# Kernel optimization log

Hardware: AMD Instinct MI355X
Metric: run time of the kernel (lower is better)

The kernel has to match this reference:

```python
import jax, jax.numpy as jnp
import numpy as np

N_NODES = 50000
N_GRAPHS = 128
IN_DIM = 512
HID = 512
N_LAYERS = 3


def setup_inputs() -> dict:
    key = jax.random.key(0)
    ks = jax.random.split(key, 12)
    inp = {
        "x": jax.random.normal(ks[0], (N_NODES, IN_DIM), dtype=jnp.float32),
        "walk2": jax.random.randint(ks[1], (3, N_NODES), 0, N_NODES, dtype=jnp.int32),
        "walk3": jax.random.randint(ks[2], (4, N_NODES), 0, N_NODES, dtype=jnp.int32),
        "walk4": jax.random.randint(ks[3], (5, N_NODES), 0, N_NODES, dtype=jnp.int32),
        "batch": jnp.sort(jax.random.randint(ks[4], (N_NODES,), 0, N_GRAPHS, dtype=jnp.int32)),
    }
    dims = [IN_DIM, HID, HID]
    for i in range(N_LAYERS):
        scale = 1.0 / np.sqrt(dims[i])
        inp[f"W{i}"] = jax.random.normal(ks[5 + i], (dims[i], HID), dtype=jnp.float32) * scale
        inp[f"b{i}"] = jnp.zeros((HID,), dtype=jnp.float32)
    return inp


def _gather_sum(z, walk):
    # walk: [L, N] node indices -> sum of gathered embeddings, [N, H]
    L, N = walk.shape
    return jnp.take(z, walk.reshape(-1), axis=0).reshape(L, N, z.shape[1]).sum(0)


def reference(x, walk2, walk3, walk4, batch, W0, b0, W1, b1, W2, b2):
    layers = [(W0, b0), (W1, b1), (W2, b2)]
    path_batch = jnp.take(batch, walk2[0])  # [N]
    counts = jax.ops.segment_sum(jnp.ones((path_batch.shape[0],), jnp.float32),
                                 path_batch, num_segments=N_GRAPHS)
    denom = jnp.maximum(counts, 1.0)[:, None]  # avoid div-by-zero for empty graphs
    z = x
    g = []
    for W, b in layers:
        z = z @ W + b  # [N, H]
        path_emb = _gather_sum(z, walk2) + _gather_sum(z, walk3) + _gather_sum(z, walk4)
        pooled = jax.ops.segment_sum(path_emb, path_batch, num_segments=N_GRAPHS) / denom
        g.append(pooled)
    return jnp.concatenate(g, axis=1)  # [N_GRAPHS, 3*H]
```

## Files before the change

kernel.cpp:

```cpp
#include <hip/hip_runtime.h>

#define N_NODES 50000
#define N_GRAPHS 128
#define HID 512

#define KSPAN   272
#define NSTEP   17
#define KS2     48
#define KSPLIT  (KS2 * 4)
#define KPAD    (KSPAN * KSPLIT)
#define NPANEL  (KPAD / 16)

#define C8_OFF     0
#define C8_BYTES   ((size_t)N_GRAPHS * KPAD)
#define PSUM_OFF   (C8_OFF + C8_BYTES)
#define PSUM_BYTES ((size_t)N_GRAPHS * HID * 4)
#define COUNTS_OFF (PSUM_OFF + PSUM_BYTES)
#define ZERO_BYTES (COUNTS_OFF + 512)
#define APACK_OFF  ZERO_BYTES
#define APACK_BYTES ((size_t)NPANEL * 4 * 64 * 16)
#define PART_OFF   (APACK_OFF + APACK_BYTES)
#define PART_BYTES ((size_t)KS2 * N_GRAPHS * HID * 4)

typedef __attribute__((ext_vector_type(8))) short bf16x8;
typedef __attribute__((ext_vector_type(16))) float f32x16;

__global__ __launch_bounds__(256)
void build_c_kernel(const int* __restrict__ w2, const int* __restrict__ w3,
                    const int* __restrict__ w4, const int* __restrict__ batch,
                    unsigned int* __restrict__ C32, int* __restrict__ counts) {
    __shared__ int hist[N_GRAPHS];
    const int t = threadIdx.x;
    if (t < N_GRAPHS) hist[t] = 0;
    __syncthreads();
    const int i = blockIdx.x * 256 + t;
    if (i < N_NODES) {
        const int a = w2[i];
        const int g = batch[a];
        atomicAdd(&hist[g], 1);
        unsigned int* row = C32 + (size_t)g * (KPAD / 4);
        int nn[12];
        nn[0]  = a;
        nn[1]  = w2[N_NODES + i];
        nn[2]  = w2[2 * N_NODES + i];
        nn[3]  = w3[i];
        nn[4]  = w3[N_NODES + i];
        nn[5]  = w3[2 * N_NODES + i];
        nn[6]  = w3[3 * N_NODES + i];
        nn[7]  = w4[i];
        nn[8]  = w4[N_NODES + i];
        nn[9]  = w4[2 * N_NODES + i];
        nn[10] = w4[3 * N_NODES + i];
        nn[11] = w4[4 * N_NODES + i];
#pragma unroll
        for (int j = 0; j < 12; ++j) {
            const int nd = nn[j];
            atomicAdd(&row[nd >> 2], 1u << ((nd & 3) * 8));
        }
    }
    __syncthreads();
    if (t < N_GRAPHS) { const int hv = hist[t]; if (hv) atomicAdd(&counts[t], hv); }
}

__device__ inline unsigned pack_bf16(unsigned a, unsigned b) {
    return (__builtin_bit_cast(unsigned, (float)a) >> 16) |
           (__builtin_bit_cast(unsigned, (float)b) & 0xFFFF0000u);
}

__global__ __launch_bounds__(256)
void c8_to_apack_kernel(const unsigned char* __restrict__ C8,
                        uint4* __restrict__ Apack) {
    const int kp = blockIdx.x;
    const int t = threadIdx.x;
    const int mt = t >> 6;
    const int l = t & 63;
    const int row = mt * 32 + (l & 31);
    const int k0 = kp * 16 + 8 * (l >> 5);
    const uint2 b = *(const uint2*)(C8 + (size_t)row * KPAD + k0);
    uint4 o;
    o.x = pack_bf16(b.x & 0xFFu, (b.x >> 8) & 0xFFu);
    o.y = pack_bf16((b.x >> 16) & 0xFFu, b.x >> 24);
    o.z = pack_bf16(b.y & 0xFFu, (b.y >> 8) & 0xFFu);
    o.w = pack_bf16((b.y >> 16) & 0xFFu, b.y >> 24);
    Apack[(size_t)(kp * 4 + mt) * 64 + l] = o;
}

template <int GUARD>
__device__ inline void issue_b8(const float* __restrict__ xp, int krow,
                                unsigned (&u)[8]) {
#pragma unroll
    for (int j = 0; j < 8; ++j) {
        int k = krow + j;
        if (GUARD) k = min(k, N_NODES - 1);
        u[j] = __builtin_bit_cast(unsigned, xp[(size_t)k * HID]);
    }
}

__device__ inline f32x16 mfma_bf16(bf16x8 a, bf16x8 b, f32x16 c) {
    return __builtin_amdgcn_mfma_f32_32x32x16_bf16(a, b, c, 0, 0, 0);
}

__device__ inline unsigned bpack(unsigned u0, unsigned u1) {
    return __builtin_amdgcn_perm(u1, u0, 0x07060302u);
}

__device__ inline void step_mfma4(const unsigned (&u)[8], const uint4 (&a)[4],
                                  f32x16 (&acc)[4]) {
    unsigned d[4];
#pragma unroll
    for (int jj = 0; jj < 4; ++jj) d[jj] = bpack(u[2 * jj], u[2 * jj + 1]);
    const bf16x8 b0 = __builtin_bit_cast(bf16x8, make_uint4(d[0], d[1], d[2], d[3]));
#pragma unroll
    for (int mt = 0; mt < 4; ++mt)
        acc[mt] = mfma_bf16(__builtin_bit_cast(bf16x8, a[mt]), b0, acc[mt]);
}

template <int GUARD>
__device__ inline void run_k4(const float* __restrict__ xp,
                              const uint4* __restrict__ Apack,
                              int kbase, int h, int lane,
                              f32x16 (&acc)[4]) {
    unsigned bu[3][8];
    uint4 au[3][4];
    const int kp0 = kbase >> 4;
#pragma unroll
    for (int s = 0; s < 3; ++s) {
        issue_b8<GUARD>(xp, kbase + s * 16 + 8 * h, bu[s]);
#pragma unroll
        for (int mt = 0; mt < 4; ++mt)
            au[s][mt] = Apack[(size_t)((kp0 + s) * 4 + mt) * 64 + lane];
    }
#pragma unroll
    for (int s = 0; s < NSTEP; ++s) {
        const int slot = s % 3;
        step_mfma4(bu[slot], au[slot], acc);
        if (s + 3 < NSTEP) {
            issue_b8<GUARD>(xp, kbase + (s + 3) * 16 + 8 * h, bu[slot]);
#pragma unroll
            for (int mt = 0; mt < 4; ++mt)
                au[slot][mt] = Apack[(size_t)((kp0 + s + 3) * 4 + mt) * 64 + lane];
        }
    }
}

template <int ATOMIC>
__global__ __launch_bounds__(256, 3)
void pool_gemm7_kernel(const float* __restrict__ x,
                       const uint4* __restrict__ Apack,
                       float* __restrict__ dst) {
    __shared__ float red[3][16 * 64];
    const int t = threadIdx.x;
    const int lane = t & 63;
    const int w = t >> 6;
    const int n = lane & 31;
    const int h = lane >> 5;
    const int rn = blockIdx.x;
    const int ks = blockIdx.y * 4 + w;
    const int kbase = ks * KSPAN;

    f32x16 acc[4];
#pragma unroll
    for (int p = 0; p < 4; ++p)
#pragma unroll
        for (int r = 0; r < 16; ++r) acc[p][r] = 0.f;

    const float* xp = x + rn * 32 + n;

    if (kbase + KSPAN <= N_NODES) {
        run_k4<0>(xp, Apack, kbase, h, lane, acc);
    } else if (kbase < N_NODES) {
        run_k4<1>(xp, Apack, kbase, h, lane, acc);
    }

    float* outp = ATOMIC ? dst : dst + (size_t)blockIdx.y * (N_GRAPHS * HID);
#pragma unroll
    for (int p = 0; p < 4; ++p) {
        __syncthreads();
        if (w > 0) {
#pragma unroll
            for (int i = 0; i < 16; ++i)
                red[w - 1][i * 64 + lane] = acc[p][i];
        }
        __syncthreads();
        if (w == 0) {
#pragma unroll
            for (int i = 0; i < 16; ++i) {
                const float v = acc[p][i] + red[0][i * 64 + lane] +
                                red[1][i * 64 + lane] + red[2][i * 64 + lane];
                const int row = p * 32 + (i & 3) + 8 * (i >> 2) + 4 * h;
                const int col = rn * 32 + n;
                if (ATOMIC) atomicAdd(&outp[(size_t)row * HID + col], v);
                else        outp[(size_t)row * HID + col] = v;
            }
        }
    }
}

__global__ __launch_bounds__(256)
void reduce_part_kernel(const float* __restrict__ part, float* __restrict__ Psum) {
    const int id = blockIdx.x * 256 + threadIdx.x;
    float s0 = 0.f, s1 = 0.f;
    for (int k = 0; k + 2 <= KS2; k += 2) {
        s0 += part[(size_t)k * (N_GRAPHS * HID) + id];
        s1 += part[(size_t)(k + 1) * (N_GRAPHS * HID) + id];
    }
    Psum[id] = s0 + s1;
}

__global__ __launch_bounds__(256)
void layer_gemm_kernel(const float* __restrict__ A, int lda, int scaleA,
                       const float* __restrict__ W,
                       const float* __restrict__ bias,
                       const int* __restrict__ counts,
                       float* __restrict__ out) {
    __shared__ float Alds[16][128];
    const int ct = blockIdx.x, rt = blockIdx.y, ksb = blockIdx.z;
    const int t = threadIdx.x;
    const int cc = ct * 64 + (t & 63);
    const int wv = t >> 6;
    const int k0 = ksb * 128;

    for (int idx = t; idx < 16 * 32; idx += 256) {
        const int rr = idx >> 5;
        const int kk = (idx & 31) * 4;
        const int row = rt * 16 + rr;
        float4 v = *(const float4*)&A[(size_t)row * lda + k0 + kk];
        if (scaleA) {
            const float inv = 1.f / (float)max(counts[row], 1);
            v.x *= inv; v.y *= inv; v.z *= inv; v.w *= inv;
        }
        *(float4*)&Alds[rr][kk] = v;
    }
    __syncthreads();

    const int r0 = rt * 16 + wv * 4;
    float a0 = 0.f, a1 = 0.f, a2 = 0.f, a3 = 0.f;
#pragma unroll 8
    for (int k = 0; k < 128; ++k) {
        const float wval = W[(size_t)(k0 + k) * HID + cc];
        a0 += Alds[wv * 4 + 0][k] * wval;
        a1 += Alds[wv * 4 + 1][k] * wval;
        a2 += Alds[wv * 4 + 2][k] * wval;
        a3 += Alds[wv * 4 + 3][k] * wval;
    }
    if (ksb == 0) {
        const float bc = bias[cc];
        a0 += (counts[r0 + 0] > 0 ? 12.f : 0.f) * bc;
        a1 += (counts[r0 + 1] > 0 ? 12.f : 0.f) * bc;
        a2 += (counts[r0 + 2] > 0 ? 12.f : 0.f) * bc;
        a3 += (counts[r0 + 3] > 0 ? 12.f : 0.f) * bc;
    }
    atomicAdd(&out[(size_t)(r0 + 0) * 1536 + cc], a0);
    atomicAdd(&out[(size_t)(r0 + 1) * 1536 + cc], a1);
    atomicAdd(&out[(size_t)(r0 + 2) * 1536 + cc], a2);
    atomicAdd(&out[(size_t)(r0 + 3) * 1536 + cc], a3);
}

extern "C" void kernel_launch(void* const* d_in, const int* in_sizes, int n_in,
                              void* d_out, int out_size, void* d_ws, size_t ws_size,
                              hipStream_t stream) {
    const float* x     = (const float*)d_in[0];
    const int*   w2    = (const int*)d_in[1];
    const int*   w3    = (const int*)d_in[2];
    const int*   w4    = (const int*)d_in[3];
    const int*   batch = (const int*)d_in[4];
    const float* W0    = (const float*)d_in[5];
    const float* b0    = (const float*)d_in[6];
    const float* W1    = (const float*)d_in[7];
    const float* b1    = (const float*)d_in[8];
    const float* W2    = (const float*)d_in[9];
    const float* b2    = (const float*)d_in[10];
    float* out = (float*)d_out;

    unsigned char* ws  = (unsigned char*)d_ws;
    unsigned int* C32  = (unsigned int*)(ws + C8_OFF);
    float* Psum        = (float*)(ws + PSUM_OFF);
    int* counts        = (int*)(ws + COUNTS_OFF);
    uint4* Apack       = (uint4*)(ws + APACK_OFF);
    float* part        = (float*)(ws + PART_OFF);
    const bool use_part = ws_size >= PART_OFF + PART_BYTES;

    hipMemsetAsync(d_ws, 0, ZERO_BYTES, stream);
    hipMemsetAsync(d_out, 0, (size_t)out_size * 4, stream);

    build_c_kernel<<<(N_NODES + 255) / 256, 256, 0, stream>>>(w2, w3, w4, batch, C32, counts);
    c8_to_apack_kernel<<<NPANEL, 256, 0, stream>>>((const unsigned char*)C32, Apack);

    if (use_part) {
        pool_gemm7_kernel<0><<<dim3(16, KS2), 256, 0, stream>>>(x, Apack, part);
        reduce_part_kernel<<<256, 256, 0, stream>>>(part, Psum);
    } else {
        pool_gemm7_kernel<1><<<dim3(16, KS2), 256, 0, stream>>>(x, Apack, Psum);
    }

    layer_gemm_kernel<<<dim3(8, 8, 4), 256, 0, stream>>>(Psum, HID, 1, W0, b0, counts, out);
    layer_gemm_kernel<<<dim3(8, 8, 4), 256, 0, stream>>>(out, 1536, 0, W1, b1, counts, out + 512);
    layer_gemm_kernel<<<dim3(8, 8, 4), 256, 0, stream>>>(out + 512, 1536, 0, W2, b2, counts, out + 1024);
}
```

Measured before the change: 268.2 us.

## Fuse pool GEMM, reduction and layer GEMMs into one cooperative kernel

Merges the pool GEMM, the partial-sum reduction, the output zeroing and the three layer GEMMs into a single cooperative kernel of 768 blocks, using grid-wide syncs in place of separate launches. The output memset moves into the kernel, running on the blocks that would otherwise sit idle during the reduction. The aim is to remove five kernel launches and their gaps. In exchange it adds grid.sync barriers, and in the layer phases only 256 of the 768 blocks do work. Co-residency of 768 blocks at 3 per CU is assumed; if the cooperative launch fails, the code falls back to the old multi-kernel path.

```diff
diff --git a/kernel.cpp b/kernel.cpp
--- a/kernel.cpp
+++ b/kernel.cpp
@@ -1,4 +1,7 @@
 #include <hip/hip_runtime.h>
+#include <hip/hip_cooperative_groups.h>
+
+namespace cg = cooperative_groups;
 
 #define N_NODES 50000
 #define N_GRAPHS 128
@@ -144,18 +147,18 @@
 }
 
 template <int ATOMIC>
-__global__ __launch_bounds__(256, 3)
-void pool_gemm7_kernel(const float* __restrict__ x,
-                       const uint4* __restrict__ Apack,
-                       float* __restrict__ dst) {
-    __shared__ float red[3][16 * 64];
-    const int t = threadIdx.x;
+__device__ inline void pool_phase(float* __restrict__ smem, int lb, int t,
+                                  const float* __restrict__ x,
+                                  const uint4* __restrict__ Apack,
+                                  float* __restrict__ dst) {
+    float (*red)[16 * 64] = (float (*)[16 * 64])smem;
     const int lane = t & 63;
     const int w = t >> 6;
     const int n = lane & 31;
     const int h = lane >> 5;
-    const int rn = blockIdx.x;
-    const int ks = blockIdx.y * 4 + w;
+    const int rn = lb & 15;
+    const int ksg = lb >> 4;
+    const int ks = ksg * 4 + w;
     const int kbase = ks * KSPAN;
 
     f32x16 acc[4];
@@ -172,7 +175,7 @@
         run_k4<1>(xp, Apack, kbase, h, lane, acc);
     }
 
-    float* outp = ATOMIC ? dst : dst + (size_t)blockIdx.y * (N_GRAPHS * HID);
+    float* outp = ATOMIC ? dst : dst + (size_t)ksg * (N_GRAPHS * HID);
 #pragma unroll
     for (int p = 0; p < 4; ++p) {
         __syncthreads();
@@ -196,9 +199,9 @@
     }
 }
 
-__global__ __launch_bounds__(256)
-void reduce_part_kernel(const float* __restrict__ part, float* __restrict__ Psum) {
-    const int id = blockIdx.x * 256 + threadIdx.x;
+__device__ inline void reduce_phase(int lb, int t, const float* __restrict__ part,
+                                    float* __restrict__ Psum) {
+    const int id = lb * 256 + t;
     float s0 = 0.f, s1 = 0.f;
     for (int k = 0; k + 2 <= KS2; k += 2) {
         s0 += part[(size_t)k * (N_GRAPHS * HID) + id];
@@ -207,15 +210,15 @@
     Psum[id] = s0 + s1;
 }
 
-__global__ __launch_bounds__(256)
-void layer_gemm_kernel(const float* __restrict__ A, int lda, int scaleA,
-                       const float* __restrict__ W,
-                       const float* __restrict__ bias,
-                       const int* __restrict__ counts,
-                       float* __restrict__ out) {
-    __shared__ float Alds[16][128];
-    const int ct = blockIdx.x, rt = blockIdx.y, ksb = blockIdx.z;
-    const int t = threadIdx.x;
+__device__ inline void layer_phase(float* __restrict__ smem, int lb, int t,
+                                   const float* __restrict__ A, int lda, int scaleA,
+                                   const float* __restrict__ W,
+                                   const float* __restrict__ bias,
+                                   const int* __restrict__ counts,
+                                   float* __restrict__ out) {
+    if (lb >= 256) return;
+    float (*Alds)[128] = (float (*)[128])smem;
+    const int ct = lb & 7, rt = (lb >> 3) & 7, ksb = lb >> 6;
     const int cc = ct * 64 + (t & 63);
     const int wv = t >> 6;
     const int k0 = ksb * 128;
@@ -254,6 +257,62 @@
     atomicAdd(&out[(size_t)(r0 + 1) * 1536 + cc], a1);
     atomicAdd(&out[(size_t)(r0 + 2) * 1536 + cc], a2);
     atomicAdd(&out[(size_t)(r0 + 3) * 1536 + cc], a3);
+    __syncthreads();
+}
+
+__global__ __launch_bounds__(256, 3)
+void fused_tail_kernel(const float* __restrict__ x, const uint4* __restrict__ Apack,
+                       float* __restrict__ part, float* __restrict__ Psum,
+                       const int* __restrict__ counts,
+                       const float* __restrict__ W0, const float* __restrict__ b0,
+                       const float* __restrict__ W1, const float* __restrict__ b1,
+                       const float* __restrict__ W2, const float* __restrict__ b2,
+                       float* __restrict__ out) {
+    __shared__ float smem[3 * 16 * 64];
+    cg::grid_group grid = cg::this_grid();
+    const int lb = blockIdx.x;
+    const int t = threadIdx.x;
+
+    pool_phase<0>(smem, lb, t, x, Apack, part);
+    grid.sync();
+
+    if (lb < 256) reduce_phase(lb, t, part, Psum);
+    else {
+        for (int idx = (lb - 256) * 256 + t; idx < N_GRAPHS * 1536; idx += 512 * 256)
+            out[idx] = 0.f;
+    }
+    grid.sync();
+
+    layer_phase(smem, lb, t, Psum, HID, 1, W0, b0, counts, out);
+    grid.sync();
+    layer_phase(smem, lb, t, out, 1536, 0, W1, b1, counts, out + 512);
+    grid.sync();
+    layer_phase(smem, lb, t, out + 512, 1536, 0, W2, b2, counts, out + 1024);
+}
+
+template <int ATOMIC>
+__global__ __launch_bounds__(256, 3)
+void pool_gemm7_kernel(const float* __restrict__ x,
+                       const uint4* __restrict__ Apack,
+                       float* __restrict__ dst) {
+    __shared__ float smem[3 * 16 * 64];
+    pool_phase<ATOMIC>(smem, blockIdx.x + 16 * blockIdx.y, threadIdx.x, x, Apack, dst);
+}
+
+__global__ __launch_bounds__(256)
+void reduce_part_kernel(const float* __restrict__ part, float* __restrict__ Psum) {
+    reduce_phase(blockIdx.x, threadIdx.x, part, Psum);
+}
+
+__global__ __launch_bounds__(256)
+void layer_gemm_kernel(const float* __restrict__ A, int lda, int scaleA,
+                       const float* __restrict__ W,
+                       const float* __restrict__ bias,
+                       const int* __restrict__ counts,
+                       float* __restrict__ out) {
+    __shared__ float smem[16 * 128];
+    layer_phase(smem, blockIdx.x + 8 * blockIdx.y + 64 * blockIdx.z, threadIdx.x,
+                A, lda, scaleA, W, bias, counts, out);
 }
 
 extern "C" void kernel_launch(void* const* d_in, const int* in_sizes, int n_in,
@@ -280,20 +339,40 @@
     float* part        = (float*)(ws + PART_OFF);
     const bool use_part = ws_size >= PART_OFF + PART_BYTES;
 
+    static int coop_ok = -1;
+    if (coop_ok < 0) {
+        int dev = 0, v = 0;
+        hipGetDevice(&dev);
+        hipDeviceGetAttribute(&v, hipDeviceAttributeCooperativeLaunch, dev);
+        coop_ok = v;
+    }
+
     hipMemsetAsync(d_ws, 0, ZERO_BYTES, stream);
-    hipMemsetAsync(d_out, 0, (size_t)out_size * 4, stream);
 
     build_c_kernel<<<(N_NODES + 255) / 256, 256, 0, stream>>>(w2, w3, w4, batch, C32, counts);
     c8_to_apack_kernel<<<NPANEL, 256, 0, stream>>>((const unsigned char*)C32, Apack);
 
-    if (use_part) {
-        pool_gemm7_kernel<0><<<dim3(16, KS2), 256, 0, stream>>>(x, Apack, part);
-        reduce_part_kernel<<<256, 256, 0, stream>>>(part, Psum);
-    } else {
-        pool_gemm7_kernel<1><<<dim3(16, KS2), 256, 0, stream>>>(x, Apack, Psum);
-    }
-
-    layer_gemm_kernel<<<dim3(8, 8, 4), 256, 0, stream>>>(Psum, HID, 1, W0, b0, counts, out);
-    layer_gemm_kernel<<<dim3(8, 8, 4), 256, 0, stream>>>(out, 1536, 0, W1, b1, counts, out + 512);
-    layer_gemm_kernel<<<dim3(8, 8, 4), 256, 0, stream>>>(out + 512, 1536, 0, W2, b2, counts, out + 1024);
-}
+    bool done = false;
+    if (use_part && coop_ok) {
+        void* args[] = {(void*)&x, (void*)&Apack, (void*)&part, (void*)&Psum,
+                        (void*)&counts, (void*)&W0, (void*)&b0, (void*)&W1,
+                        (void*)&b1, (void*)&W2, (void*)&b2, (void*)&out};
+        hipError_t err = hipLaunchCooperativeKernel(
+            reinterpret_cast<void*>(fused_tail_kernel), dim3(16 * KS2), dim3(256),
+            args, 0, stream);
+        done = (err == hipSuccess);
+    }
+
+    if (!done) {
+        hipMemsetAsync(d_out, 0, (size_t)out_size * 4, stream);
+        if (use_part) {
+            pool_gemm7_kernel<0><<<dim3(16, KS2), 256, 0, stream>>>(x, Apack, part);
+            reduce_part_kernel<<<256, 256, 0, stream>>>(part, Psum);
+        } else {
+            pool_gemm7_kernel<1><<<dim3(16, KS2), 256, 0, stream>>>(x, Apack, Psum);
+        }
+        layer_gemm_kernel<<<dim3(8, 8, 4), 256, 0, stream>>>(Psum, HID, 1, W0, b0, counts, out);
+        layer_gemm_kernel<<<dim3(8, 8, 4), 256, 0, stream>>>(out, 1536, 0, W1, b1, counts, out + 512);
+        layer_gemm_kernel<<<dim3(8, 8, 4), 256, 0, stream>>>(out + 512, 1536, 0, W2, b2, counts, out + 1024);
+    }
+}
```

Result: slower. 616.5 us (+129.9%).
